# Optimization experiments

Measured on AMD Instinct MI355X. Metric: run time of the kernel, lower is better.

The kernel has to match this reference:

```python
import jax, jax.numpy as jnp
import numpy as np

N_NODES = 100000
N_EDGES = 1600000
D_IN = 128
D_HID = 128
D_OUT = 40
N_LAYERS = 3
EPS = 1e-12


def setup_inputs() -> dict:
    key = jax.random.key(0)
    ks = jax.random.split(key, 12)
    s = 1.0 / np.sqrt(D_HID)
    return {
        "x": jax.random.normal(ks[0], (N_NODES, D_IN), jnp.float32),
        "edge_index": jax.random.randint(ks[1], (2, N_EDGES), 0, N_NODES, jnp.int64),
        "Wl": jax.random.uniform(ks[2], (N_LAYERS, D_HID, D_HID), jnp.float32, -s, s),
        "bl": jax.random.uniform(ks[3], (N_LAYERS, D_HID), jnp.float32, -s, s),
        "Wr": jax.random.uniform(ks[4], (N_LAYERS, D_HID, D_HID), jnp.float32, -s, s),
        "br": jax.random.uniform(ks[5], (N_LAYERS, D_HID), jnp.float32, -s, s),
        "W_post1": jax.random.uniform(ks[6], (D_HID, D_HID), jnp.float32, -s, s),
        "b_post1": jax.random.uniform(ks[7], (D_HID,), jnp.float32, -s, s),
        "W_post2": jax.random.uniform(ks[8], (D_OUT, D_HID), jnp.float32, -s, s),
        "b_post2": jax.random.uniform(ks[9], (D_OUT,), jnp.float32, -s, s),
    }


def reference(x, edge_index, Wl, bl, Wr, br, W_post1, b_post1, W_post2, b_post2):
    src, dst = edge_index[0], edge_index[1]
    n = x.shape[0]
    h = x
    for i in range(N_LAYERS):
        # scatter-add aggregation of neighbor features (MessagePassing aggr='add')
        prop = jax.ops.segment_sum(h[src], dst, num_segments=n)  # [N, D]
        out = h @ Wl[i].T + bl[i] + prop @ Wr[i].T + br[i]
        # F.normalize(out, p=2) along dim=1
        norm = jnp.linalg.norm(out, axis=1, keepdims=True)
        out = out / jnp.maximum(norm, EPS)
        h = jax.nn.relu(out)  # dropout p=0 -> identity
    h = h @ W_post1.T + b_post1
    h = h @ W_post2.T + b_post2
    return jax.nn.log_softmax(h, axis=1)
```

## Files before the change

kernel.cpp:

```cpp
#include <hip/hip_runtime.h>
#include <hip/hip_bf16.h>
#include <cstdint>
#include <cstddef>

#define NN 100000
#define DD 128
#define NE 1600000
#define NPB 196
#define NBUCK 511
#define BCAP 6144
#define BUCKCAP 4608
#define SCHUNK 8192

typedef short bf16x8 __attribute__((ext_vector_type(8)));
typedef float f32x4 __attribute__((ext_vector_type(4)));
typedef unsigned short u16;
typedef unsigned int u32;

__device__ inline float b2f(u16 u) {
    union { u32 i; float f; } c; c.i = ((u32)u) << 16; return c.f;
}
__device__ inline u16 f2b(float f) {
    __hip_bfloat16 h = __float2bfloat16(f);
    return *reinterpret_cast<u16*>(&h);
}

__global__ __launch_bounds__(256)
void initcur_kernel(int* __restrict__ cur) {
    int t = blockIdx.x * 256 + threadIdx.x;
    if (t < NBUCK) cur[t] = t * BUCKCAP;
}

__global__ __launch_bounds__(256)
void bscatter_kernel(const int* __restrict__ ei, int* __restrict__ cursor,
                     u32* __restrict__ packed, int n_edges) {
    __shared__ int hist[NBUCK];
    const int tid = threadIdx.x;
    const int nchunks = (n_edges + SCHUNK - 1) / SCHUNK;
    for (int ch = blockIdx.x; ch < nchunks; ch += gridDim.x) {
        const int e0 = ch * SCHUNK;
        const int e1 = min(e0 + SCHUNK, n_edges);
        for (int i = tid; i < NBUCK; i += 256) hist[i] = 0;
        __syncthreads();
        for (int e = e0 + tid; e < e1; e += 256)
            atomicAdd(&hist[ei[n_edges + e] / NPB], 1);
        __syncthreads();
        for (int i = tid; i < NBUCK; i += 256) {
            int c = hist[i];
            hist[i] = (c > 0) ? atomicAdd(&cursor[i], c) : 0;
        }
        __syncthreads();
        for (int e = e0 + tid; e < e1; e += 256) {
            int s = ei[e];
            int d = ei[n_edges + e];
            int b = d / NPB;
            int ld = d - b * NPB;
            int pos = atomicAdd(&hist[b], 1);
            packed[pos] = ((u32)ld << 17) | (u32)s;
        }
        __syncthreads();
    }
}

__global__ __launch_bounds__(256)
void blocal_kernel(const u32* __restrict__ packed, const int* __restrict__ cursor,
                   int* __restrict__ row_ptr, int* __restrict__ rpe,
                   int* __restrict__ ssrc) {
    __shared__ int out_s[BCAP];
    __shared__ int cur_s[NPB];
    __shared__ int excl_s[NPB];
    __shared__ int ws[4];
    __shared__ int wexc[4];

    const int b = blockIdx.x;
    const int tid = threadIdx.x;
    const int lane = tid & 63, wv = tid >> 6;
    const int pbase = b * BUCKCAP;
    const int cnt = cursor[b] - pbase;

    if (tid < NPB) cur_s[tid] = 0;
    __syncthreads();
    for (int i = tid; i < cnt; i += 256)
        atomicAdd(&cur_s[packed[pbase + i] >> 17], 1);
    __syncthreads();

    int v = (tid < NPB) ? cur_s[tid] : 0;
    int inc = v;
    #pragma unroll
    for (int o = 1; o < 64; o <<= 1) {
        int u = __shfl_up(inc, o);
        if (lane >= o) inc += u;
    }
    if (lane == 63) ws[wv] = inc;
    __syncthreads();
    if (tid == 0) {
        int s = 0;
        #pragma unroll
        for (int k = 0; k < 4; ++k) { wexc[k] = s; s += ws[k]; }
    }
    __syncthreads();
    int excl = inc - v + wexc[wv];
    if (tid < NPB) excl_s[tid] = excl;
    int gnode = b * NPB + tid;
    if (tid < NPB && gnode < NN) {
        row_ptr[gnode] = pbase + excl;
        rpe[gnode] = pbase + excl + v;
    }
    __syncthreads();
    if (tid < NPB) cur_s[tid] = excl_s[tid];
    __syncthreads();

    if (cnt <= BCAP) {
        for (int i = tid; i < cnt; i += 256) {
            u32 p = packed[pbase + i];
            int pos = atomicAdd(&cur_s[p >> 17], 1);
            out_s[pos] = (int)(p & 0x1FFFF);
        }
        __syncthreads();
        for (int i = tid; i < cnt; i += 256) ssrc[pbase + i] = out_s[i];
    } else {
        for (int i = tid; i < cnt; i += 256) {
            u32 p = packed[pbase + i];
            int pos = atomicAdd(&cur_s[p >> 17], 1);
            ssrc[pbase + pos] = (int)(p & 0x1FFFF);
        }
    }
}

__global__ __launch_bounds__(256)
void cvt_x_kernel(const float* __restrict__ x, u16* __restrict__ xb, long long n4) {
    long long t = (long long)blockIdx.x * blockDim.x + threadIdx.x;
    long long stride = (long long)gridDim.x * blockDim.x;
    for (; t < n4; t += stride) {
        float4 v = reinterpret_cast<const float4*>(x)[t];
        ushort4 o;
        o.x = f2b(v.x); o.y = f2b(v.y); o.z = f2b(v.z); o.w = f2b(v.w);
        reinterpret_cast<ushort4*>(xb)[t] = o;
    }
}

__global__ __launch_bounds__(256)
void cvt_w_kernel(const float* __restrict__ Wl, const float* __restrict__ Wr,
                  u16* __restrict__ Wcat) {
    int t = blockIdx.x * blockDim.x + threadIdx.x;
    const int NCAT = 3 * 128 * 256;
    if (t < NCAT) {
        int layer = t >> 15;
        int rem = t & 32767;
        int d = rem >> 8;
        int k = rem & 255;
        float v = (k < 128) ? Wl[layer * 16384 + d * 128 + k]
                            : Wr[layer * 16384 + d * 128 + (k - 128)];
        Wcat[t] = f2b(v);
    }
}

__global__ __launch_bounds__(256)
void wfuse_kernel(const float* __restrict__ W1f, const float* __restrict__ b1,
                  const float* __restrict__ W2, const float* __restrict__ b2,
                  u16* __restrict__ Wfb, float* __restrict__ bfuse) {
    int t = blockIdx.x * 256 + threadIdx.x;
    if (t < 48 * 128) {
        int l = t >> 7, k = t & 127;
        float s = 0.0f;
        if (l < 40) {
            for (int j = 0; j < 128; ++j)
                s += W2[l * 128 + j] * W1f[j * 128 + k];
        }
        Wfb[t] = f2b(s);
    }
    if (blockIdx.x == 0 && threadIdx.x < 40) {
        int l = threadIdx.x;
        float s = b2[l];
        for (int j = 0; j < 128; ++j) s += W2[l * 128 + j] * b1[j];
        bfuse[l] = s;
    }
}

#define ACC8(v) do { \
    union { u32 i; float f; } _c; \
    _c.i = (v).x << 16;          acc0 += _c.f; \
    _c.i = (v).x & 0xffff0000u;  acc1 += _c.f; \
    _c.i = (v).y << 16;          acc2 += _c.f; \
    _c.i = (v).y & 0xffff0000u;  acc3 += _c.f; \
    _c.i = (v).z << 16;          acc4 += _c.f; \
    _c.i = (v).z & 0xffff0000u;  acc5 += _c.f; \
    _c.i = (v).w << 16;          acc6 += _c.f; \
    _c.i = (v).w & 0xffff0000u;  acc7 += _c.f; \
} while (0)

__global__ __launch_bounds__(256)
void gather_kernel(const u16* __restrict__ h, const int* __restrict__ rp,
                   const int* __restrict__ rpe, const int* __restrict__ ssrc,
                   u16* __restrict__ prop, int n_nodes) {
    int wid = (blockIdx.x * blockDim.x + threadIdx.x) >> 6;
    int lane = threadIdx.x & 63;
    if (wid >= n_nodes) return;
    int beg = rp[wid], end = rpe[wid];
    int deg = end - beg;
    int nb = min(deg, 64);
    const int g = lane >> 4;
    const u16* hb = h + (lane & 15) * 8;

    float acc0 = 0, acc1 = 0, acc2 = 0, acc3 = 0;
    float acc4 = 0, acc5 = 0, acc6 = 0, acc7 = 0;

    int sv = (lane < nb) ? ssrc[beg + lane] : 0;

    int j = 0;
    for (; j + 15 < nb; j += 16) {
        int s0 = __shfl(sv, j + g);
        int s1 = __shfl(sv, j + 4 + g);
        int s2 = __shfl(sv, j + 8 + g);
        int s3 = __shfl(sv, j + 12 + g);
        uint4 v0 = *reinterpret_cast<const uint4*>(hb + (size_t)s0 * DD);
        uint4 v1 = *reinterpret_cast<const uint4*>(hb + (size_t)s1 * DD);
        uint4 v2 = *reinterpret_cast<const uint4*>(hb + (size_t)s2 * DD);
        uint4 v3 = *reinterpret_cast<const uint4*>(hb + (size_t)s3 * DD);
        ACC8(v0);
        ACC8(v1);
        ACC8(v2);
        ACC8(v3);
    }
    for (; j + 7 < nb; j += 8) {
        int s0 = __shfl(sv, j + g);
        int s1 = __shfl(sv, j + 4 + g);
        uint4 v0 = *reinterpret_cast<const uint4*>(hb + (size_t)s0 * DD);
        uint4 v1 = *reinterpret_cast<const uint4*>(hb + (size_t)s1 * DD);
        ACC8(v0);
        ACC8(v1);
    }
    for (; j + 3 < nb; j += 4) {
        int s0 = __shfl(sv, j + g);
        uint4 v0 = *reinterpret_cast<const uint4*>(hb + (size_t)s0 * DD);
        ACC8(v0);
    }
    if (j < nb && g < nb - j) {
        int s0 = __shfl(sv, j + g);
        uint4 v0 = *reinterpret_cast<const uint4*>(hb + (size_t)s0 * DD);
        ACC8(v0);
    }
    for (int e = beg + 64 + g; e < end; e += 4) {
        int s0 = ssrc[e];
        uint4 v0 = *reinterpret_cast<const uint4*>(hb + (size_t)s0 * DD);
        ACC8(v0);
    }

    acc0 += __shfl_xor(acc0, 16); acc0 += __shfl_xor(acc0, 32);
    acc1 += __shfl_xor(acc1, 16); acc1 += __shfl_xor(acc1, 32);
    acc2 += __shfl_xor(acc2, 16); acc2 += __shfl_xor(acc2, 32);
    acc3 += __shfl_xor(acc3, 16); acc3 += __shfl_xor(acc3, 32);
    acc4 += __shfl_xor(acc4, 16); acc4 += __shfl_xor(acc4, 32);
    acc5 += __shfl_xor(acc5, 16); acc5 += __shfl_xor(acc5, 32);
    acc6 += __shfl_xor(acc6, 16); acc6 += __shfl_xor(acc6, 32);
    acc7 += __shfl_xor(acc7, 16); acc7 += __shfl_xor(acc7, 32);

    if (lane < 16) {
        uint4 o;
        o.x = (u32)f2b(acc0) | ((u32)f2b(acc1) << 16);
        o.y = (u32)f2b(acc2) | ((u32)f2b(acc3) << 16);
        o.z = (u32)f2b(acc4) | ((u32)f2b(acc5) << 16);
        o.w = (u32)f2b(acc6) | ((u32)f2b(acc7) << 16);
        *reinterpret_cast<uint4*>(prop + (size_t)wid * DD + lane * 8) = o;
    }
}

__global__ __launch_bounds__(256)
void mfma_layer64(const u16* __restrict__ hin, const u16* __restrict__ prop,
                  const u16* __restrict__ Wc, const float* __restrict__ b1,
                  const float* __restrict__ b2, u16* __restrict__ out,
                  int n_nodes) {
    __shared__ char a_s[64 * 512];
    __shared__ float red_s[64][4];

    const int tid = threadIdx.x;
    const int w = tid >> 6;
    const int l = tid & 63;
    const int q = l >> 4;
    const int c16 = l & 15;

    bf16x8 bfrag[2][8];
    int col[2];
    float bias[2];
    #pragma unroll
    for (int t = 0; t < 2; ++t) {
        col[t] = w * 32 + t * 16 + c16;
        bias[t] = b1[col[t]] + b2[col[t]];
        #pragma unroll
        for (int kk = 0; kk < 8; ++kk)
            bfrag[t][kk] = *reinterpret_cast<const bf16x8*>(
                Wc + (size_t)col[t] * 256 + kk * 32 + q * 8);
    }

    const int base = blockIdx.x * 64;

    for (int ci = tid; ci < 2048; ci += 256) {
        int r = ci >> 5, c = ci & 31;
        int node = base + r;
        uint4 v = {0, 0, 0, 0};
        if (node < n_nodes) {
            const u16* src = (c < 16) ? (hin + (size_t)node * DD + c * 8)
                                      : (prop + (size_t)node * DD + (c - 16) * 8);
            v = *reinterpret_cast<const uint4*>(src);
        }
        *reinterpret_cast<uint4*>(a_s + r * 512 + ((c ^ (r & 7)) * 16)) = v;
    }
    __syncthreads();

    f32x4 acc[4][2] = {};
    #pragma unroll
    for (int kk = 0; kk < 8; ++kk) {
        int cc = kk * 4 + q;
        #pragma unroll
        for (int m = 0; m < 4; ++m) {
            int row = m * 16 + c16;
            bf16x8 a = *reinterpret_cast<const bf16x8*>(
                a_s + row * 512 + ((cc ^ (row & 7)) * 16));
            acc[m][0] = __builtin_amdgcn_mfma_f32_16x16x32_bf16(a, bfrag[0][kk], acc[m][0], 0, 0, 0);
            acc[m][1] = __builtin_amdgcn_mfma_f32_16x16x32_bf16(a, bfrag[1][kk], acc[m][1], 0, 0, 0);
        }
    }

    float vals[4][2][4];
    float ss[4][4];
    #pragma unroll
    for (int m = 0; m < 4; ++m) {
        #pragma unroll
        for (int reg = 0; reg < 4; ++reg) {
            float s = 0.0f;
            #pragma unroll
            for (int t = 0; t < 2; ++t) {
                float v = acc[m][t][reg] + bias[t];
                vals[m][t][reg] = v;
                s += v * v;
            }
            s += __shfl_xor(s, 1);
            s += __shfl_xor(s, 2);
            s += __shfl_xor(s, 4);
            s += __shfl_xor(s, 8);
            ss[m][reg] = s;
        }
    }
    if (c16 == 0) {
        #pragma unroll
        for (int m = 0; m < 4; ++m)
            #pragma unroll
            for (int reg = 0; reg < 4; ++reg)
                red_s[m * 16 + q * 4 + reg][w] = ss[m][reg];
    }
    __syncthreads();
    #pragma unroll
    for (int m = 0; m < 4; ++m) {
        #pragma unroll
        for (int reg = 0; reg < 4; ++reg) {
            int row = m * 16 + q * 4 + reg;
            float4 rr = *reinterpret_cast<float4*>(&red_s[row][0]);
            float tot = rr.x + rr.y + rr.z + rr.w;
            float rn = 1.0f / fmaxf(sqrtf(tot), 1e-12f);
            if (base + row < n_nodes) {
                #pragma unroll
                for (int t = 0; t < 2; ++t) {
                    float v = fmaxf(vals[m][t][reg] * rn, 0.0f);
                    out[(size_t)(base + row) * DD + col[t]] = f2b(v);
                }
            }
        }
    }
}

__global__ __launch_bounds__(256)
void postfused_kernel(const u16* __restrict__ hin, const u16* __restrict__ Wfb,
                      const float* __restrict__ bfuse, float* __restrict__ out,
                      int n_nodes) {
    __shared__ char a_s[64 * 256];
    const int tid = threadIdx.x;
    const int w = tid >> 6;
    const int l = tid & 63;
    const int q = l >> 4;
    const int c16 = l & 15;

    bf16x8 bfrag[3][4];
    float bias[3];
    int col[3];
    #pragma unroll
    for (int t = 0; t < 3; ++t) {
        col[t] = t * 16 + c16;
        bias[t] = (col[t] < 40) ? bfuse[col[t]] : 0.0f;
        #pragma unroll
        for (int kk = 0; kk < 4; ++kk)
            bfrag[t][kk] = *reinterpret_cast<const bf16x8*>(
                Wfb + col[t] * 128 + kk * 32 + q * 8);
    }

    const int base = blockIdx.x * 64;

    for (int ci = tid; ci < 1024; ci += 256) {
        int r = ci >> 4, c = ci & 15;
        uint4 v = {0, 0, 0, 0};
        if (base + r < n_nodes)
            v = *reinterpret_cast<const uint4*>(hin + (size_t)(base + r) * DD + c * 8);
        *reinterpret_cast<uint4*>(a_s + r * 256 + ((c ^ (r & 7)) * 16)) = v;
    }
    __syncthreads();

    f32x4 acc[3] = {};
    const int arow = w * 16 + c16;
    #pragma unroll
    for (int kk = 0; kk < 4; ++kk) {
        int cc = kk * 4 + q;
        bf16x8 a = *reinterpret_cast<const bf16x8*>(
            a_s + arow * 256 + ((cc ^ (arow & 7)) * 16));
        acc[0] = __builtin_amdgcn_mfma_f32_16x16x32_bf16(a, bfrag[0][kk], acc[0], 0, 0, 0);
        acc[1] = __builtin_amdgcn_mfma_f32_16x16x32_bf16(a, bfrag[1][kk], acc[1], 0, 0, 0);
        acc[2] = __builtin_amdgcn_mfma_f32_16x16x32_bf16(a, bfrag[2][kk], acc[2], 0, 0, 0);
    }

    #pragma unroll
    for (int reg = 0; reg < 4; ++reg) {
        int row = base + w * 16 + q * 4 + reg;
        float v[3];
        float m = -INFINITY;
        #pragma unroll
        for (int t = 0; t < 3; ++t) {
            v[t] = acc[t][reg] + bias[t];
            if (col[t] < 40) m = fmaxf(m, v[t]);
        }
        m = fmaxf(m, __shfl_xor(m, 1));
        m = fmaxf(m, __shfl_xor(m, 2));
        m = fmaxf(m, __shfl_xor(m, 4));
        m = fmaxf(m, __shfl_xor(m, 8));
        float s = 0.0f;
        #pragma unroll
        for (int t = 0; t < 3; ++t)
            if (col[t] < 40) s += expf(v[t] - m);
        s += __shfl_xor(s, 1);
        s += __shfl_xor(s, 2);
        s += __shfl_xor(s, 4);
        s += __shfl_xor(s, 8);
        float lg = logf(s);
        if (row < n_nodes) {
            #pragma unroll
            for (int t = 0; t < 3; ++t)
                if (col[t] < 40)
                    out[(size_t)row * 40 + col[t]] = v[t] - m - lg;
        }
    }
}

extern "C" void kernel_launch(void* const* d_in, const int* in_sizes, int n_in,
                              void* d_out, int out_size, void* d_ws, size_t ws_size,
                              hipStream_t stream) {
    const float* x   = (const float*)d_in[0];
    const int*   ei  = (const int*)d_in[1];
    const float* Wl  = (const float*)d_in[2];
    const float* bl  = (const float*)d_in[3];
    const float* Wr  = (const float*)d_in[4];
    const float* br  = (const float*)d_in[5];
    const float* W1f = (const float*)d_in[6];
    const float* b1  = (const float*)d_in[7];
    const float* W2  = (const float*)d_in[8];
    const float* b2  = (const float*)d_in[9];
    float* outp = (float*)d_out;

    u16* xb   = (u16*)d_ws;
    u16* P    = xb + (size_t)NN * DD;
    u16* bufA = P + (size_t)NN * DD;
    u16* bufB = bufA + (size_t)NN * DD;
    u16* Wcat = bufB + (size_t)NN * DD;
    u16* Wfb  = Wcat + 3 * 128 * 256;
    float* bfuse = (float*)(Wfb + 8192);
    int* cursor  = (int*)(Wfb + 128 * 128);
    int* row_ptr = cursor + NBUCK + 1;
    int* rpe     = row_ptr + NN;
    int* ssrc    = rpe + NN;
    u32* packed  = (u32*)(ssrc + NBUCK * BUCKCAP);

    initcur_kernel<<<2, 256, 0, stream>>>(cursor);
    bscatter_kernel<<<(NE + SCHUNK - 1) / SCHUNK, 256, 0, stream>>>(
        ei, cursor, packed, NE);
    blocal_kernel<<<NBUCK, 256, 0, stream>>>(packed, cursor, row_ptr, rpe, ssrc);

    cvt_x_kernel<<<12500, 256, 0, stream>>>(x, xb, (long long)NN * DD / 4);
    cvt_w_kernel<<<(3 * 128 * 256 + 255) / 256, 256, 0, stream>>>(Wl, Wr, Wcat);
    wfuse_kernel<<<24, 256, 0, stream>>>(W1f, b1, W2, b2, Wfb, bfuse);

    const int n_strips64 = (NN + 63) / 64;
    const int gather_grid = (NN * 64 + 255) / 256;

    const u16* hcur = xb;
    u16* hnext;
    for (int i = 0; i < 3; ++i) {
        hnext = (i == 0) ? bufA : ((hcur == bufA) ? bufB : bufA);
        gather_kernel<<<gather_grid, 256, 0, stream>>>(
            hcur, row_ptr, rpe, ssrc, P, NN);
        mfma_layer64<<<n_strips64, 256, 0, stream>>>(
            hcur, P, Wcat + (size_t)i * 128 * 256,
            bl + (size_t)i * DD, br + (size_t)i * DD, hnext, NN);
        hcur = hnext;
    }
    postfused_kernel<<<n_strips64, 256, 0, stream>>>(hcur, Wfb, bfuse, outp, NN);
}
```

Baseline: 344.3 us.

## Gather neighbor features from an FP8 copy of node features

Keeps an FP8 copy of the node features, written alongside the bf16 conversion of x and refreshed after each layer by a new conversion kernel. The neighbor-sum gather then reads 8-byte FP8 rows instead of 16-byte bf16 rows, halving the random-access gather traffic. In exchange it adds a conversion pass per layer and loses precision in the aggregated features, which may affect accuracy. It also drops the 8-wide tail loop from the bf16 gather.

```diff
diff --git a/kernel.cpp b/kernel.cpp
--- a/kernel.cpp
+++ b/kernel.cpp
@@ -12,10 +12,20 @@
 #define BUCKCAP 4608
 #define SCHUNK 8192
 
+#if defined(__has_builtin)
+# if __has_builtin(__builtin_amdgcn_cvt_pk_f32_fp8) && __has_builtin(__builtin_amdgcn_cvt_pk_fp8_f32)
+#  define HAS_FP8 1
+# endif
+#endif
+#ifndef HAS_FP8
+# define HAS_FP8 0
+#endif
+
 typedef short bf16x8 __attribute__((ext_vector_type(8)));
 typedef float f32x4 __attribute__((ext_vector_type(4)));
 typedef unsigned short u16;
 typedef unsigned int u32;
+typedef unsigned char u8;
 
 __device__ inline float b2f(u16 u) {
     union { u32 i; float f; } c; c.i = ((u32)u) << 16; return c.f;
@@ -24,6 +34,15 @@
     __hip_bfloat16 h = __float2bfloat16(f);
     return *reinterpret_cast<u16*>(&h);
 }
+
+#if HAS_FP8
+__device__ inline u32 pack4_fp8(float a, float b, float c, float d) {
+    u32 r = 0;
+    r = (u32)__builtin_amdgcn_cvt_pk_fp8_f32(a, b, (int)r, false);
+    r = (u32)__builtin_amdgcn_cvt_pk_fp8_f32(c, d, (int)r, true);
+    return r;
+}
+#endif
 
 __global__ __launch_bounds__(256)
 void initcur_kernel(int* __restrict__ cur) {
@@ -128,16 +147,48 @@
 }
 
 __global__ __launch_bounds__(256)
-void cvt_x_kernel(const float* __restrict__ x, u16* __restrict__ xb, long long n4) {
+void cvt_x_kernel(const float* __restrict__ x, u16* __restrict__ xb,
+                  u8* __restrict__ x8, long long n8) {
     long long t = (long long)blockIdx.x * blockDim.x + threadIdx.x;
     long long stride = (long long)gridDim.x * blockDim.x;
-    for (; t < n4; t += stride) {
-        float4 v = reinterpret_cast<const float4*>(x)[t];
-        ushort4 o;
-        o.x = f2b(v.x); o.y = f2b(v.y); o.z = f2b(v.z); o.w = f2b(v.w);
-        reinterpret_cast<ushort4*>(xb)[t] = o;
-    }
-}
+    for (; t < n8; t += stride) {
+        float4 v0 = reinterpret_cast<const float4*>(x)[2 * t];
+        float4 v1 = reinterpret_cast<const float4*>(x)[2 * t + 1];
+        uint4 ob;
+        ob.x = (u32)f2b(v0.x) | ((u32)f2b(v0.y) << 16);
+        ob.y = (u32)f2b(v0.z) | ((u32)f2b(v0.w) << 16);
+        ob.z = (u32)f2b(v1.x) | ((u32)f2b(v1.y) << 16);
+        ob.w = (u32)f2b(v1.z) | ((u32)f2b(v1.w) << 16);
+        reinterpret_cast<uint4*>(xb)[t] = ob;
+#if HAS_FP8
+        uint2 o8;
+        o8.x = pack4_fp8(v0.x, v0.y, v0.z, v0.w);
+        o8.y = pack4_fp8(v1.x, v1.y, v1.z, v1.w);
+        reinterpret_cast<uint2*>(x8)[t] = o8;
+#endif
+    }
+}
+
+#if HAS_FP8
+__global__ __launch_bounds__(256)
+void cvt8_kernel(const u16* __restrict__ hb, u8* __restrict__ h8, int n8) {
+    int t0 = blockIdx.x * 256 + threadIdx.x;
+    int stride = gridDim.x * 256;
+    for (int t = t0; t < n8; t += stride) {
+        uint4 v = reinterpret_cast<const uint4*>(hb)[t];
+        union { u32 i; float f; } c;
+        float f0, f1, f2, f3, f4, f5, f6, f7;
+        c.i = v.x << 16; f0 = c.f;  c.i = v.x & 0xffff0000u; f1 = c.f;
+        c.i = v.y << 16; f2 = c.f;  c.i = v.y & 0xffff0000u; f3 = c.f;
+        c.i = v.z << 16; f4 = c.f;  c.i = v.z & 0xffff0000u; f5 = c.f;
+        c.i = v.w << 16; f6 = c.f;  c.i = v.w & 0xffff0000u; f7 = c.f;
+        uint2 o;
+        o.x = pack4_fp8(f0, f1, f2, f3);
+        o.y = pack4_fp8(f4, f5, f6, f7);
+        reinterpret_cast<uint2*>(h8)[t] = o;
+    }
+}
+#endif
 
 __global__ __launch_bounds__(256)
 void cvt_w_kernel(const float* __restrict__ Wl, const float* __restrict__ Wr,
@@ -177,6 +228,85 @@
     }
 }
 
+#if HAS_FP8
+#define DEC8(q) do { \
+    auto _p0 = __builtin_amdgcn_cvt_pk_f32_fp8((q).x, false); \
+    auto _p1 = __builtin_amdgcn_cvt_pk_f32_fp8((q).x, true); \
+    auto _p2 = __builtin_amdgcn_cvt_pk_f32_fp8((q).y, false); \
+    auto _p3 = __builtin_amdgcn_cvt_pk_f32_fp8((q).y, true); \
+    acc0 += _p0[0]; acc1 += _p0[1]; acc2 += _p1[0]; acc3 += _p1[1]; \
+    acc4 += _p2[0]; acc5 += _p2[1]; acc6 += _p3[0]; acc7 += _p3[1]; \
+} while (0)
+
+__global__ __launch_bounds__(256)
+void gather8_kernel(const u8* __restrict__ h8, const int* __restrict__ rp,
+                    const int* __restrict__ rpe, const int* __restrict__ ssrc,
+                    u16* __restrict__ prop, int n_nodes) {
+    int wid = (blockIdx.x * blockDim.x + threadIdx.x) >> 6;
+    int lane = threadIdx.x & 63;
+    if (wid >= n_nodes) return;
+    int beg = rp[wid], end = rpe[wid];
+    int deg = end - beg;
+    int nb = min(deg, 64);
+    const int g = lane >> 4;
+    const u8* hb = h8 + (lane & 15) * 8;
+
+    float acc0 = 0, acc1 = 0, acc2 = 0, acc3 = 0;
+    float acc4 = 0, acc5 = 0, acc6 = 0, acc7 = 0;
+
+    int sv = (lane < nb) ? ssrc[beg + lane] : 0;
+
+    int j = 0;
+    for (; j + 15 < nb; j += 16) {
+        int s0 = __shfl(sv, j + g);
+        int s1 = __shfl(sv, j + 4 + g);
+        int s2 = __shfl(sv, j + 8 + g);
+        int s3 = __shfl(sv, j + 12 + g);
+        uint2 v0 = *reinterpret_cast<const uint2*>(hb + (size_t)s0 * 128);
+        uint2 v1 = *reinterpret_cast<const uint2*>(hb + (size_t)s1 * 128);
+        uint2 v2 = *reinterpret_cast<const uint2*>(hb + (size_t)s2 * 128);
+        uint2 v3 = *reinterpret_cast<const uint2*>(hb + (size_t)s3 * 128);
+        DEC8(v0);
+        DEC8(v1);
+        DEC8(v2);
+        DEC8(v3);
+    }
+    for (; j + 3 < nb; j += 4) {
+        int s0 = __shfl(sv, j + g);
+        uint2 v0 = *reinterpret_cast<const uint2*>(hb + (size_t)s0 * 128);
+        DEC8(v0);
+    }
+    if (j < nb && g < nb - j) {
+        int s0 = __shfl(sv, j + g);
+        uint2 v0 = *reinterpret_cast<const uint2*>(hb + (size_t)s0 * 128);
+        DEC8(v0);
+    }
+    for (int e = beg + 64 + g; e < end; e += 4) {
+        int s0 = ssrc[e];
+        uint2 v0 = *reinterpret_cast<const uint2*>(hb + (size_t)s0 * 128);
+        DEC8(v0);
+    }
+
+    acc0 += __shfl_xor(acc0, 16); acc0 += __shfl_xor(acc0, 32);
+    acc1 += __shfl_xor(acc1, 16); acc1 += __shfl_xor(acc1, 32);
+    acc2 += __shfl_xor(acc2, 16); acc2 += __shfl_xor(acc2, 32);
+    acc3 += __shfl_xor(acc3, 16); acc3 += __shfl_xor(acc3, 32);
+    acc4 += __shfl_xor(acc4, 16); acc4 += __shfl_xor(acc4, 32);
+    acc5 += __shfl_xor(acc5, 16); acc5 += __shfl_xor(acc5, 32);
+    acc6 += __shfl_xor(acc6, 16); acc6 += __shfl_xor(acc6, 32);
+    acc7 += __shfl_xor(acc7, 16); acc7 += __shfl_xor(acc7, 32);
+
+    if (lane < 16) {
+        uint4 o;
+        o.x = (u32)f2b(acc0) | ((u32)f2b(acc1) << 16);
+        o.y = (u32)f2b(acc2) | ((u32)f2b(acc3) << 16);
+        o.z = (u32)f2b(acc4) | ((u32)f2b(acc5) << 16);
+        o.w = (u32)f2b(acc6) | ((u32)f2b(acc7) << 16);
+        *reinterpret_cast<uint4*>(prop + (size_t)wid * DD + lane * 8) = o;
+    }
+}
+#endif
+
 #define ACC8(v) do { \
     union { u32 i; float f; } _c; \
     _c.i = (v).x << 16;          acc0 += _c.f; \
@@ -190,9 +320,9 @@
 } while (0)
 
 __global__ __launch_bounds__(256)
-void gather_kernel(const u16* __restrict__ h, const int* __restrict__ rp,
-                   const int* __restrict__ rpe, const int* __restrict__ ssrc,
-                   u16* __restrict__ prop, int n_nodes) {
+void gatherb_kernel(const u16* __restrict__ h, const int* __restrict__ rp,
+                    const int* __restrict__ rpe, const int* __restrict__ ssrc,
+                    u16* __restrict__ prop, int n_nodes) {
     int wid = (blockIdx.x * blockDim.x + threadIdx.x) >> 6;
     int lane = threadIdx.x & 63;
     if (wid >= n_nodes) return;
@@ -222,14 +352,6 @@
         ACC8(v2);
         ACC8(v3);
     }
-    for (; j + 7 < nb; j += 8) {
-        int s0 = __shfl(sv, j + g);
-        int s1 = __shfl(sv, j + 4 + g);
-        uint4 v0 = *reinterpret_cast<const uint4*>(hb + (size_t)s0 * DD);
-        uint4 v1 = *reinterpret_cast<const uint4*>(hb + (size_t)s1 * DD);
-        ACC8(v0);
-        ACC8(v1);
-    }
     for (; j + 3 < nb; j += 4) {
         int s0 = __shfl(sv, j + g);
         uint4 v0 = *reinterpret_cast<const uint4*>(hb + (size_t)s0 * DD);
@@ -466,7 +588,8 @@
     u16* P    = xb + (size_t)NN * DD;
     u16* bufA = P + (size_t)NN * DD;
     u16* bufB = bufA + (size_t)NN * DD;
-    u16* Wcat = bufB + (size_t)NN * DD;
+    u8*  h8   = (u8*)(bufB + (size_t)NN * DD);
+    u16* Wcat = (u16*)(h8 + (size_t)NN * 128);
     u16* Wfb  = Wcat + 3 * 128 * 256;
     float* bfuse = (float*)(Wfb + 8192);
     int* cursor  = (int*)(Wfb + 128 * 128);
@@ -480,22 +603,32 @@
         ei, cursor, packed, NE);
     blocal_kernel<<<NBUCK, 256, 0, stream>>>(packed, cursor, row_ptr, rpe, ssrc);
 
-    cvt_x_kernel<<<12500, 256, 0, stream>>>(x, xb, (long long)NN * DD / 4);
+    cvt_x_kernel<<<6250, 256, 0, stream>>>(x, xb, h8, (long long)NN * DD / 8);
     cvt_w_kernel<<<(3 * 128 * 256 + 255) / 256, 256, 0, stream>>>(Wl, Wr, Wcat);
     wfuse_kernel<<<24, 256, 0, stream>>>(W1f, b1, W2, b2, Wfb, bfuse);
 
     const int n_strips64 = (NN + 63) / 64;
     const int gather_grid = (NN * 64 + 255) / 256;
+    const int n8 = NN * DD / 8;
 
     const u16* hcur = xb;
     u16* hnext;
     for (int i = 0; i < 3; ++i) {
         hnext = (i == 0) ? bufA : ((hcur == bufA) ? bufB : bufA);
-        gather_kernel<<<gather_grid, 256, 0, stream>>>(
+#if HAS_FP8
+        gather8_kernel<<<gather_grid, 256, 0, stream>>>(
+            h8, row_ptr, rpe, ssrc, P, NN);
+#else
+        gatherb_kernel<<<gather_grid, 256, 0, stream>>>(
             hcur, row_ptr, rpe, ssrc, P, NN);
+#endif
         mfma_layer64<<<n_strips64, 256, 0, stream>>>(
             hcur, P, Wcat + (size_t)i * 128 * 256,
             bl + (size_t)i * DD, br + (size_t)i * DD, hnext, NN);
+#if HAS_FP8
+        if (i < 2)
+            cvt8_kernel<<<2048, 256, 0, stream>>>(hnext, h8, n8);
+#endif
         hcur = hnext;
     }
     postfused_kernel<<<n_strips64, 256, 0, stream>>>(hcur, Wfb, bfuse, outp, NN);
```

Measured after the change: 346.3 us. Within noise of the previous version (+0.6%).
